# Kernel tuning notes

Measured on AMD Instinct MI355X. Metric: run time of the kernel, lower is better.

Reference implementation:

```python
import jax, jax.numpy as jnp
import numpy as np

B, N, MAX_DEG = 256, 512, 6
F_IN, H = 62, 128  # layers = [62, 128, 128]
NUM_DEG = MAX_DEG + 1  # degree buckets 0..6


def gather_neighbors(atoms, edges, maskvalue):
    # atoms [B,N,F], edges [B,N,D] with -1 padding -> [B,N,D,F]
    idx = jnp.maximum(edges, 0)
    neigh = jax.vmap(lambda a, e: a[e])(atoms, idx)
    return jnp.where(edges[..., None] < 0, jnp.asarray(maskvalue, atoms.dtype), neigh)


def nfp_conv(atoms, edges, W, b):
    # W [NUM_DEG, F_in, F_out], b [NUM_DEG, F_out]
    deg = jnp.sum(edges >= 0, axis=-1)  # [B,N]
    neigh = gather_neighbors(atoms, edges, 0.0)
    summed = neigh.sum(axis=2) + atoms  # include self, [B,N,F_in]
    out = jnp.zeros(summed.shape[:2] + (W.shape[-1],), summed.dtype)
    for d in range(NUM_DEG):  # small fixed set of degree buckets
        h = jax.nn.sigmoid(summed @ W[d] + b[d])
        out = out + h * (deg == d)[..., None].astype(h.dtype)
    return out


def graph_pool(atoms, edges):
    # max over self + neighbors
    neigh = gather_neighbors(atoms, edges, -jnp.inf)
    allf = jnp.concatenate([atoms[:, :, None, :], neigh], axis=2)  # [B,N,D+1,F]
    return allf.max(axis=2)


def setup_inputs() -> dict:
    key = jax.random.key(0)
    ka, ke, km, k0, k1, k2, k3 = jax.random.split(key, 7)
    a = jax.random.normal(ka, (B, N, F_IN), dtype=jnp.float32)
    e = jax.random.randint(ke, (B, N, MAX_DEG), 0, N, dtype=jnp.int32)
    # introduce -1 padding so atoms have varied degrees 0..6
    u = jax.random.uniform(km, (B, N, MAX_DEG))
    e = jnp.where(u < 0.6, e, -1).astype(jnp.int32)
    W0 = jax.random.normal(k0, (NUM_DEG, F_IN, H), dtype=jnp.float32) * 0.1
    b0 = jax.random.normal(k1, (NUM_DEG, H), dtype=jnp.float32) * 0.1
    W1 = jax.random.normal(k2, (NUM_DEG, H, H), dtype=jnp.float32) * 0.1
    b1 = jax.random.normal(k3, (NUM_DEG, H), dtype=jnp.float32) * 0.1
    return {"a": a, "e": e, "W0": W0, "b0": b0, "W1": W1, "b1": b1}


def reference(a, e, W0, b0, W1, b1):
    x = nfp_conv(a, e, W0, b0)
    x = graph_pool(x, e)
    x = nfp_conv(x, e, W1, b1)
    x = graph_pool(x, e)
    return x.sum(axis=1)  # SubgraphSum: [B, H]
```

## Files before the change

kernel.cpp:

```cpp
#include <hip/hip_runtime.h>
#include <math.h>

#define BB 256
#define NN 512
#define DD 6
#define F_IN 62
#define HH 128
#define ND 7
#define TOTAL (BB*NN)
#define G8 8
#define NG 32
#define GOPB 5120
#define MAXSG (NG*GOPB)
#define T128 (MAXSG/128)
#define T64  (MAXSG/64)
#define STG 132

typedef __bf16 bf16x8 __attribute__((ext_vector_type(8)));
typedef float f32x4 __attribute__((ext_vector_type(4)));

__device__ __forceinline__ unsigned short f2bf(float f) {
    unsigned u = __builtin_bit_cast(unsigned, f);
    u = (u + 0x7FFFu + ((u >> 16) & 1u)) >> 16;
    return (unsigned short)u;
}
__device__ __forceinline__ float lo2f(unsigned x) { return __builtin_bit_cast(float, x << 16); }
__device__ __forceinline__ float hi2f(unsigned x) { return __builtin_bit_cast(float, x & 0xFFFF0000u); }

__device__ __forceinline__ uint4 pack8(const float* s) {
    uint4 r;
    r.x = (unsigned)f2bf(s[0]) | ((unsigned)f2bf(s[1]) << 16);
    r.y = (unsigned)f2bf(s[2]) | ((unsigned)f2bf(s[3]) << 16);
    r.z = (unsigned)f2bf(s[4]) | ((unsigned)f2bf(s[5]) << 16);
    r.w = (unsigned)f2bf(s[6]) | ((unsigned)f2bf(s[7]) << 16);
    return r;
}
__device__ __forceinline__ void unpack_add(float* s, uint4 q) {
    s[0] += lo2f(q.x); s[1] += hi2f(q.x); s[2] += lo2f(q.y); s[3] += hi2f(q.y);
    s[4] += lo2f(q.z); s[5] += hi2f(q.z); s[6] += lo2f(q.w); s[7] += hi2f(q.w);
}
__device__ __forceinline__ void unpack_max(float* s, uint4 q) {
    s[0] = fmaxf(s[0], lo2f(q.x)); s[1] = fmaxf(s[1], hi2f(q.x));
    s[2] = fmaxf(s[2], lo2f(q.y)); s[3] = fmaxf(s[3], hi2f(q.y));
    s[4] = fmaxf(s[4], lo2f(q.z)); s[5] = fmaxf(s[5], hi2f(q.z));
    s[6] = fmaxf(s[6], lo2f(q.w)); s[7] = fmaxf(s[7], hi2f(q.w));
}
__device__ __forceinline__ void rowadd62(float* s, const float* r, int kb) {
    float2 z0 = *(const float2*)(r);     s[0] += z0.x; s[1] += z0.y;
    float2 z1 = *(const float2*)(r + 2); s[2] += z1.x; s[3] += z1.y;
    float2 z2 = *(const float2*)(r + 4); s[4] += z2.x; s[5] += z2.y;
    if (kb < 7) { float2 z3 = *(const float2*)(r + 6); s[6] += z3.x; s[7] += z3.y; }
}


__global__ __launch_bounds__(512) void k_hist(const int* __restrict__ e,
                                              int* __restrict__ deg,
                                              int* __restrict__ cnt) {
    __shared__ unsigned int lh[ND];
    const int b = blockIdx.x;
    const int t = threadIdx.x;
    if (t < ND) lh[t] = 0u;
    __syncthreads();
    int d = 0;
#pragma unroll
    for (int j = 0; j < DD; ++j) d += (e[(b * NN + t) * DD + j] >= 0) ? 1 : 0;
    deg[b * NN + t] = d;
    atomicAdd(&lh[d], 1u);
    __syncthreads();
    if (t < ND) cnt[b * 8 + t] = (int)lh[t];
}


__global__ __launch_bounds__(256) void k_scan_grp(const int* __restrict__ cnt,
                                                  int* __restrict__ base_bd,
                                                  int* __restrict__ tdeg64) {
    __shared__ int lc[BB * 8];
    __shared__ int bnd[NG][8];
    const int t = threadIdx.x;
    for (int i = t; i < BB * 8; i += 256) lc[i] = cnt[i];
    __syncthreads();
    if (t < NG) {
        int acc = t * GOPB;
        for (int d = 0; d < ND; ++d) {
            bnd[t][d] = acc;
            for (int b8 = 0; b8 < G8; ++b8) {
                int b = t * G8 + b8;
                base_bd[b * 8 + d] = acc;
                acc += lc[b * 8 + d];
            }
            acc = (acc + 127) & ~127;
        }
        bnd[t][7] = acc;
    }
    __syncthreads();
    for (int i = t; i < T64; i += 256) {
        int g = i / (GOPB / 64);
        int s = i * 64;
        int dd = 0;
        if (s < bnd[g][7]) {
            for (int d = ND - 1; d >= 0; --d) if (s >= bnd[g][d]) { dd = d; break; }
        }
        tdeg64[i] = dd;
    }
}

__global__ __launch_bounds__(512) void k_init_order(int* __restrict__ order) {
    order[blockIdx.x * 512 + threadIdx.x] = -1;
}

__global__ __launch_bounds__(512) void k_scatter(const int* __restrict__ deg,
                                                 const int* __restrict__ base_bd,
                                                 int* __restrict__ order) {
    __shared__ unsigned int rk[ND];
    const int b = blockIdx.x;
    const int t = threadIdx.x;
    if (t < ND) rk[t] = 0u;
    __syncthreads();
    const int u = b * NN + t;
    const int d = deg[u];
    unsigned r = atomicAdd(&rk[d], 1u);
    order[base_bd[b * 8 + d] + (int)r] = u;
}


__global__ void k_prep_wt(const float* __restrict__ W, unsigned short* __restrict__ WT,
                          int F, int K) {
    int n = blockIdx.x;
    int d = blockIdx.y;
    for (int k = threadIdx.x; k < K; k += 64) {
        float v = (k < F) ? W[((size_t)d * F + k) * HH + n] : 0.f;
        WT[((size_t)d * HH + n) * K + k] = f2bf(v);
    }
}


__global__ __launch_bounds__(512, 6)
void k_conv1(const float* __restrict__ a, const int* __restrict__ e,
             const unsigned short* __restrict__ WT, const float* __restrict__ bias,
             const int* __restrict__ order, const int* __restrict__ tdeg64,
             unsigned short* __restrict__ Y) {
    extern __shared__ char smem[];
    unsigned short* Wl = (unsigned short*)smem;
    unsigned short* sA = (unsigned short*)(smem + 16384);
    unsigned short* stg = sA;
    __shared__ int vT[128];

    const int t = threadIdx.x;
    const int l = t & 63;
    const int w = t >> 6;
    const int lr = l & 15;
    const int lq = l >> 4;

    const int x8 = blockIdx.x & 7;
    const int kk0 = blockIdx.x >> 3;
    const int g = x8 * 4 + kk0 / 40;
    const int tile = g * 40 + (kk0 % 40);

    if (order[tile * 128] < 0) return;
    const int d = tdeg64[tile * 2];

    if (t < 128) vT[t] = order[tile * 128 + t];
    for (int u = t; u < 1024; u += 512) {
        const int col = u >> 3, kb = u & 7;
        *(uint4*)&Wl[(col * 8 + (kb ^ (col & 7))) * 8] =
            *(const uint4*)(WT + ((size_t)d * HH + col) * 64 + kb * 8);
    }
    __syncthreads();

    for (int u = t; u < 1024; u += 512) {
        const int n = u >> 3, kb = u & 7;
        const int v = vT[n];
        float s[8] = {0.f, 0.f, 0.f, 0.f, 0.f, 0.f, 0.f, 0.f};
        if (v >= 0) {
            const int nb = v & ~(NN - 1);
            const int* ep = e + (size_t)v * DD;
            rowadd62(s, a + (size_t)v * F_IN + kb * 8, kb);
#pragma unroll
            for (int jj = 0; jj < DD; ++jj) {
                int idx = ep[jj];
                if (idx >= 0) rowadd62(s, a + (size_t)(nb + idx) * F_IN + kb * 8, kb);
            }
        }
        *(uint4*)&sA[(n * 8 + (kb ^ (n & 7))) * 8] = pack8(s);
    }
    __syncthreads();

    const int nrow = w * 16 + lr;
    bf16x8 af[2];
    af[0] = *(const bf16x8*)&sA[(nrow * 8 + ((0 + lq) ^ (nrow & 7))) * 8];
    af[1] = *(const bf16x8*)&sA[(nrow * 8 + ((4 + lq) ^ (nrow & 7))) * 8];

    f32x4 acc[8];
#pragma unroll
    for (int fr = 0; fr < 8; ++fr) {
        const int col = fr * 16 + lr;
        f32x4 z = {0.f, 0.f, 0.f, 0.f};
#pragma unroll
        for (int kk = 0; kk < 2; ++kk) {
            bf16x8 bfr = *(const bf16x8*)&Wl[(col * 8 + ((4 * kk + lq) ^ (col & 7))) * 8];
            z = __builtin_amdgcn_mfma_f32_16x16x32_bf16(af[kk], bfr, z, 0, 0, 0);
        }
        acc[fr] = z;
    }

    __syncthreads();
#pragma unroll
    for (int fr = 0; fr < 8; ++fr) {
        const int col = fr * 16 + lr;
        const float bv = bias[d * HH + col];
#pragma unroll
        for (int r2 = 0; r2 < 4; ++r2) {
            float zz = 1.f / (1.f + __expf(-(acc[fr][r2] + bv)));
            stg[(w * 16 + lq * 4 + r2) * STG + col] = f2bf(zz);
        }
    }
    __syncthreads();
    for (int u = t; u < 2048; u += 512) {
        const int n = u >> 4, c8 = (u & 15) * 8;
        const int v = vT[n];
        if (v >= 0)
            *(uint4*)&Y[(size_t)v * HH + c8] = *(const uint4*)&stg[n * STG + c8];
    }
}


__global__ __launch_bounds__(512, 6)
void k_conv2(const unsigned short* __restrict__ P1, const int* __restrict__ e,
             const unsigned short* __restrict__ WT, const float* __restrict__ bias,
             const int* __restrict__ order, const int* __restrict__ tdeg64,
             unsigned short* __restrict__ Y) {
    extern __shared__ char smem[];
    unsigned short* Wl = (unsigned short*)smem;
    unsigned short* sA = (unsigned short*)(smem + 32768);
    unsigned short* stg = sA;
    __shared__ int vT[64];

    const int t = threadIdx.x;
    const int l = t & 63;
    const int w = t >> 6;
    const int lr = l & 15;
    const int lq = l >> 4;

    const int x8 = blockIdx.x & 7;
    const int kk0 = blockIdx.x >> 3;
    const int g = x8 * 4 + kk0 / 80;
    const int tile = g * 80 + (kk0 % 80);

    if (order[tile * 64] < 0) return;
    const int d = tdeg64[tile];

    if (t < 64) vT[t] = order[tile * 64 + t];
    for (int u = t; u < 2048; u += 512) {
        const int col = u >> 4, kb = u & 15;
        *(uint4*)&Wl[(col * 16 + (kb ^ (col & 7))) * 8] =
            *(const uint4*)(WT + ((size_t)d * HH + col) * 128 + kb * 8);
    }
    __syncthreads();

    for (int u = t; u < 1024; u += 512) {
        const int n = u >> 4, kb = u & 15;
        const int v = vT[n];
        float s[8] = {0.f, 0.f, 0.f, 0.f, 0.f, 0.f, 0.f, 0.f};
        if (v >= 0) {
            const int nb = v & ~(NN - 1);
            const int* ep = e + (size_t)v * DD;
            const unsigned short* base = P1 + kb * 8;
            unpack_add(s, *(const uint4*)(base + (size_t)v * HH));
#pragma unroll
            for (int jj = 0; jj < DD; ++jj) {
                int idx = ep[jj];
                if (idx >= 0) unpack_add(s, *(const uint4*)(base + (size_t)(nb + idx) * HH));
            }
        }
        *(uint4*)&sA[(n * 16 + (kb ^ (n & 7))) * 8] = pack8(s);
    }
    __syncthreads();

    const int nrow = (w & 3) * 16 + lr;
    const int ch = w >> 2;
    bf16x8 af[4];
#pragma unroll
    for (int kk = 0; kk < 4; ++kk)
        af[kk] = *(const bf16x8*)&sA[(nrow * 16 + ((4 * kk + lq) ^ (nrow & 7))) * 8];

    f32x4 acc[4];
#pragma unroll
    for (int fr = 0; fr < 4; ++fr) {
        const int col = ch * 64 + fr * 16 + lr;
        f32x4 z = {0.f, 0.f, 0.f, 0.f};
#pragma unroll
        for (int kk = 0; kk < 4; ++kk) {
            bf16x8 bfr = *(const bf16x8*)&Wl[(col * 16 + ((4 * kk + lq) ^ (col & 7))) * 8];
            z = __builtin_amdgcn_mfma_f32_16x16x32_bf16(af[kk], bfr, z, 0, 0, 0);
        }
        acc[fr] = z;
    }

    __syncthreads();
#pragma unroll
    for (int fr = 0; fr < 4; ++fr) {
        const int col = ch * 64 + fr * 16 + lr;
        const float bv = bias[d * HH + col];
#pragma unroll
        for (int r2 = 0; r2 < 4; ++r2) {
            float zz = 1.f / (1.f + __expf(-(acc[fr][r2] + bv)));
            stg[((w & 3) * 16 + lq * 4 + r2) * STG + col] = f2bf(zz);
        }
    }
    __syncthreads();
    for (int u = t; u < 1024; u += 512) {
        const int n = u >> 4, c8 = (u & 15) * 8;
        const int v = vT[n];
        if (v >= 0)
            *(uint4*)&Y[(size_t)v * HH + c8] = *(const uint4*)&stg[n * STG + c8];
    }
}


__global__ __launch_bounds__(256) void k_pool_bf(const unsigned short* __restrict__ X,
                                                 const int* __restrict__ e,
                                                 unsigned short* __restrict__ P) {
    const int t = threadIdx.x;
    const int u = blockIdx.x * 16 + (t >> 4);
    const int c8 = (t & 15) * 8;
    const int nb = u & ~(NN - 1);
    float m[8];
    {
        uint4 p = *(const uint4*)(X + (size_t)u * HH + c8);
        m[0] = lo2f(p.x); m[1] = hi2f(p.x); m[2] = lo2f(p.y); m[3] = hi2f(p.y);
        m[4] = lo2f(p.z); m[5] = hi2f(p.z); m[6] = lo2f(p.w); m[7] = hi2f(p.w);
    }
#pragma unroll
    for (int jj = 0; jj < DD; ++jj) {
        int idx = e[u * DD + jj];
        if (idx >= 0) unpack_max(m, *(const uint4*)(X + (size_t)(nb + idx) * HH + c8));
    }
    *(uint4*)&P[(size_t)u * HH + c8] = pack8(m);
}


__global__ __launch_bounds__(256) void k_pool_sum_part(const unsigned short* __restrict__ X,
                                                       const int* __restrict__ e,
                                                       float* __restrict__ partial) {
    __shared__ float red[16][HH + 4];
    const int t = threadIdx.x;
    const int b = blockIdx.x >> 5;
    const int chunk = blockIdx.x & 31;
    const int slot = t >> 4;
    const int c8 = (t & 15) * 8;

    const int u = b * NN + chunk * 16 + slot;
    float m[8];
    {
        uint4 p = *(const uint4*)(X + (size_t)u * HH + c8);
        m[0] = lo2f(p.x); m[1] = hi2f(p.x); m[2] = lo2f(p.y); m[3] = hi2f(p.y);
        m[4] = lo2f(p.z); m[5] = hi2f(p.z); m[6] = lo2f(p.w); m[7] = hi2f(p.w);
    }
#pragma unroll
    for (int jj = 0; jj < DD; ++jj) {
        int idx = e[u * DD + jj];
        if (idx >= 0) unpack_max(m, *(const uint4*)(X + (size_t)(b * NN + idx) * HH + c8));
    }
#pragma unroll
    for (int i = 0; i < 8; ++i) red[slot][c8 + i] = m[i];
    __syncthreads();
    if (t < HH) {
        float s = 0.f;
#pragma unroll
        for (int k = 0; k < 16; ++k) s += red[k][t];
        partial[((size_t)b * 32 + chunk) * HH + t] = s;
    }
}

__global__ __launch_bounds__(256) void k_sum_final(const float* __restrict__ partial,
                                                   float* __restrict__ out) {
    int g = blockIdx.x * 256 + threadIdx.x;
    int b = g >> 7;
    int c = g & 127;
    float s = 0.f;
#pragma unroll
    for (int k = 0; k < 32; ++k) s += partial[((size_t)b * 32 + k) * HH + c];
    out[g] = s;
}


extern "C" void kernel_launch(void* const* d_in, const int* in_sizes, int n_in,
                              void* d_out, int out_size, void* d_ws, size_t ws_size,
                              hipStream_t stream) {
    const float* a  = (const float*)d_in[0];
    const int*   e  = (const int*)d_in[1];
    const float* W0 = (const float*)d_in[2];
    const float* b0 = (const float*)d_in[3];
    const float* W1 = (const float*)d_in[4];
    const float* b1 = (const float*)d_in[5];
    float* out = (float*)d_out;

    char* ws = (char*)d_ws;
    const size_t SB = (size_t)TOTAL * HH * 2;
    unsigned short* bufH = (unsigned short*)ws;
    unsigned short* bufP = (unsigned short*)(ws + SB);
    float* partial = (float*)bufP;
    char* dp = ws + 2 * SB;
    unsigned short* WT0 = (unsigned short*)dp;
    unsigned short* WT1 = WT0 + (size_t)ND * HH * 64;
    int* order   = (int*)(WT1 + (size_t)ND * HH * 128);
    int* deg     = order + MAXSG;
    int* cnt     = deg + TOTAL;
    int* base_bd = cnt + BB * 8;
    int* tdeg64  = base_bd + BB * 8;

    hipLaunchKernelGGL(k_hist, dim3(BB), dim3(NN), 0, stream, e, deg, cnt);
    hipLaunchKernelGGL(k_scan_grp, dim3(1), dim3(256), 0, stream, cnt, base_bd, tdeg64);
    hipLaunchKernelGGL(k_init_order, dim3(MAXSG / 512), dim3(512), 0, stream, order);
    hipLaunchKernelGGL(k_scatter, dim3(BB), dim3(NN), 0, stream, deg, base_bd, order);
    hipLaunchKernelGGL(k_prep_wt, dim3(HH, ND), dim3(64), 0, stream, W0, WT0, F_IN, 64);
    hipLaunchKernelGGL(k_prep_wt, dim3(HH, ND), dim3(64), 0, stream, W1, WT1, HH, HH);

    const int lds1 = 16384 + 128 * STG * 2;
    const int lds2 = 32768 + 64 * STG * 2;

    hipLaunchKernelGGL(k_conv1, dim3(T128), dim3(512), lds1, stream,
                       a, e, WT0, b0, order, tdeg64, bufH);
    hipLaunchKernelGGL(k_pool_bf, dim3(TOTAL / 16), dim3(256), 0, stream, bufH, e, bufP);
    hipLaunchKernelGGL(k_conv2, dim3(T64), dim3(512), lds2, stream,
                       bufP, e, WT1, b1, order, tdeg64, bufH);
    hipLaunchKernelGGL(k_pool_sum_part, dim3(BB * 32), dim3(256), 0, stream, bufH, e, partial);
    hipLaunchKernelGGL(k_sum_final, dim3(BB * HH / 256), dim3(256), 0, stream, partial, out);
}
```

Before: 165.1 us.

## Split neighbor gather out of conv GEMMs and merge sort preprocessing kernels

The fused gather+GEMM conv kernels are split into separate gather kernels, which write summed rows in sorted order to a workspace buffer, and GEMM kernels, which load their A fragments straight from that buffer. The four sort and histogram preprocessing kernels are merged into one per-group kernel using LDS atomics, and the two weight-prep launches are combined into one. The aim is to free the GEMM kernels from latency-bound gathers and LDS staging, and to cut launch count. In exchange, the gathered intermediate makes an extra round trip through global memory and two more launches are added.

```diff
diff --git a/kernel.cpp b/kernel.cpp
--- a/kernel.cpp
+++ b/kernel.cpp
@@ -12,8 +12,8 @@
 #define NG 32
 #define GOPB 5120
 #define MAXSG (NG*GOPB)
-#define T128 (MAXSG/128)
-#define T64  (MAXSG/64)
+#define T128G 40
+#define T64G 80
 #define STG 132
 
 typedef __bf16 bf16x8 __attribute__((ext_vector_type(8)));
@@ -53,96 +53,131 @@
 }
 
 
-__global__ __launch_bounds__(512) void k_hist(const int* __restrict__ e,
-                                              int* __restrict__ deg,
-                                              int* __restrict__ cnt) {
-    __shared__ unsigned int lh[ND];
-    const int b = blockIdx.x;
+__global__ __launch_bounds__(1024)
+void k_sort_grp(const int* __restrict__ e, int* __restrict__ order,
+                int* __restrict__ tdeg64) {
+    __shared__ int cnt[G8][8];
+    __shared__ int base[G8][8];
+    __shared__ int bnd[8];
+    __shared__ short degl[G8 * NN];
+    const int g = blockIdx.x;
     const int t = threadIdx.x;
-    if (t < ND) lh[t] = 0u;
-    __syncthreads();
-    int d = 0;
-#pragma unroll
-    for (int j = 0; j < DD; ++j) d += (e[(b * NN + t) * DD + j] >= 0) ? 1 : 0;
-    deg[b * NN + t] = d;
-    atomicAdd(&lh[d], 1u);
-    __syncthreads();
-    if (t < ND) cnt[b * 8 + t] = (int)lh[t];
-}
-
-
-__global__ __launch_bounds__(256) void k_scan_grp(const int* __restrict__ cnt,
-                                                  int* __restrict__ base_bd,
-                                                  int* __restrict__ tdeg64) {
-    __shared__ int lc[BB * 8];
-    __shared__ int bnd[NG][8];
-    const int t = threadIdx.x;
-    for (int i = t; i < BB * 8; i += 256) lc[i] = cnt[i];
-    __syncthreads();
-    if (t < NG) {
-        int acc = t * GOPB;
+    if (t < 64) ((int*)cnt)[t] = 0;
+    for (int i = t; i < GOPB; i += 1024) order[g * GOPB + i] = -1;
+    __syncthreads();
+#pragma unroll
+    for (int q = 0; q < 4; ++q) {
+        const int n = q * 1024 + t;
+        const int b8 = n >> 9, nn = n & (NN - 1);
+        const int u = (g * G8 + b8) * NN + nn;
+        int d = 0;
+#pragma unroll
+        for (int j = 0; j < DD; ++j) d += (e[u * DD + j] >= 0) ? 1 : 0;
+        degl[n] = (short)d;
+        atomicAdd(&cnt[b8][d], 1);
+    }
+    __syncthreads();
+    if (t == 0) {
+        int acc = g * GOPB;
         for (int d = 0; d < ND; ++d) {
-            bnd[t][d] = acc;
-            for (int b8 = 0; b8 < G8; ++b8) {
-                int b = t * G8 + b8;
-                base_bd[b * 8 + d] = acc;
-                acc += lc[b * 8 + d];
-            }
+            bnd[d] = acc;
+            for (int b8 = 0; b8 < G8; ++b8) { base[b8][d] = acc; acc += cnt[b8][d]; }
             acc = (acc + 127) & ~127;
         }
-        bnd[t][7] = acc;
-    }
-    __syncthreads();
-    for (int i = t; i < T64; i += 256) {
-        int g = i / (GOPB / 64);
-        int s = i * 64;
+        bnd[7] = acc;
+    }
+    __syncthreads();
+    for (int i = t; i < T64G; i += 1024) {
+        const int s = g * GOPB + i * 64;
         int dd = 0;
-        if (s < bnd[g][7]) {
-            for (int d = ND - 1; d >= 0; --d) if (s >= bnd[g][d]) { dd = d; break; }
+        if (s < bnd[7]) {
+            for (int d = ND - 1; d >= 0; --d) if (s >= bnd[d]) { dd = d; break; }
         }
-        tdeg64[i] = dd;
-    }
-}
-
-__global__ __launch_bounds__(512) void k_init_order(int* __restrict__ order) {
-    order[blockIdx.x * 512 + threadIdx.x] = -1;
-}
-
-__global__ __launch_bounds__(512) void k_scatter(const int* __restrict__ deg,
-                                                 const int* __restrict__ base_bd,
-                                                 int* __restrict__ order) {
-    __shared__ unsigned int rk[ND];
-    const int b = blockIdx.x;
-    const int t = threadIdx.x;
-    if (t < ND) rk[t] = 0u;
-    __syncthreads();
-    const int u = b * NN + t;
-    const int d = deg[u];
-    unsigned r = atomicAdd(&rk[d], 1u);
-    order[base_bd[b * 8 + d] + (int)r] = u;
-}
-
-
-__global__ void k_prep_wt(const float* __restrict__ W, unsigned short* __restrict__ WT,
-                          int F, int K) {
-    int n = blockIdx.x;
-    int d = blockIdx.y;
-    for (int k = threadIdx.x; k < K; k += 64) {
-        float v = (k < F) ? W[((size_t)d * F + k) * HH + n] : 0.f;
-        WT[((size_t)d * HH + n) * K + k] = f2bf(v);
-    }
+        tdeg64[g * T64G + i] = dd;
+    }
+    __syncthreads();
+#pragma unroll
+    for (int q = 0; q < 4; ++q) {
+        const int n = q * 1024 + t;
+        const int b8 = n >> 9, nn = n & (NN - 1);
+        const int slot = atomicAdd(&base[b8][degl[n]], 1);
+        order[slot] = (g * G8 + b8) * NN + nn;
+    }
+}
+
+
+__global__ void k_prep_w2(const float* __restrict__ W0, unsigned short* __restrict__ WT0,
+                          const float* __restrict__ W1, unsigned short* __restrict__ WT1) {
+    const int n = blockIdx.x;
+    const int d = blockIdx.y;
+    for (int k = threadIdx.x; k < 64; k += 64) {
+        float v = (k < F_IN) ? W0[((size_t)d * F_IN + k) * HH + n] : 0.f;
+        WT0[((size_t)d * HH + n) * 64 + k] = f2bf(v);
+    }
+    for (int k = threadIdx.x; k < 128; k += 64)
+        WT1[((size_t)d * HH + n) * 128 + k] = f2bf(W1[((size_t)d * HH + k) * HH + n]);
+}
+
+
+__global__ __launch_bounds__(512)
+void k_gather1(const float* __restrict__ a, const int* __restrict__ e,
+               const int* __restrict__ order, unsigned short* __restrict__ S1) {
+    const int bi = blockIdx.x;
+    const int x8 = bi & 7;
+    const int r = bi >> 3;
+    const int g = x8 * 4 + r / 80;
+    const int blk = r % 80;
+    const int slot = g * GOPB + blk * 64 + (threadIdx.x >> 3);
+    const int kb = threadIdx.x & 7;
+    const int v = order[slot];
+    if (v < 0) return;
+    const int* ep = e + (size_t)v * DD;
+    const int nb = v & ~(NN - 1);
+    float s[8] = {0.f, 0.f, 0.f, 0.f, 0.f, 0.f, 0.f, 0.f};
+    rowadd62(s, a + (size_t)v * F_IN + kb * 8, kb);
+#pragma unroll
+    for (int jj = 0; jj < DD; ++jj) {
+        int idx = ep[jj];
+        if (idx >= 0) rowadd62(s, a + (size_t)(nb + idx) * F_IN + kb * 8, kb);
+    }
+    *(uint4*)(S1 + (size_t)slot * 64 + kb * 8) = pack8(s);
+}
+
+
+__global__ __launch_bounds__(512)
+void k_gather2(const unsigned short* __restrict__ P1, const int* __restrict__ e,
+               const int* __restrict__ order, unsigned short* __restrict__ S2) {
+    const int bi = blockIdx.x;
+    const int x8 = bi & 7;
+    const int r = bi >> 3;
+    const int g = x8 * 4 + r / 160;
+    const int blk = r % 160;
+    const int slot = g * GOPB + blk * 32 + (threadIdx.x >> 4);
+    const int kb = threadIdx.x & 15;
+    const int v = order[slot];
+    if (v < 0) return;
+    const int* ep = e + (size_t)v * DD;
+    const int nb = v & ~(NN - 1);
+    const unsigned short* base = P1 + kb * 8;
+    float s[8] = {0.f, 0.f, 0.f, 0.f, 0.f, 0.f, 0.f, 0.f};
+    unpack_add(s, *(const uint4*)(base + (size_t)v * HH));
+#pragma unroll
+    for (int jj = 0; jj < DD; ++jj) {
+        int idx = ep[jj];
+        if (idx >= 0) unpack_add(s, *(const uint4*)(base + (size_t)(nb + idx) * HH));
+    }
+    *(uint4*)(S2 + (size_t)slot * HH + kb * 8) = pack8(s);
 }
 
 
 __global__ __launch_bounds__(512, 6)
-void k_conv1(const float* __restrict__ a, const int* __restrict__ e,
+void k_gemm1(const unsigned short* __restrict__ S,
              const unsigned short* __restrict__ WT, const float* __restrict__ bias,
              const int* __restrict__ order, const int* __restrict__ tdeg64,
              unsigned short* __restrict__ Y) {
     extern __shared__ char smem[];
-    unsigned short* Wl = (unsigned short*)smem;
-    unsigned short* sA = (unsigned short*)(smem + 16384);
-    unsigned short* stg = sA;
+    unsigned short* Wl  = (unsigned short*)smem;
+    unsigned short* stg = (unsigned short*)(smem + 16384);
     __shared__ int vT[128];
 
     const int t = threadIdx.x;
@@ -151,15 +186,21 @@
     const int lr = l & 15;
     const int lq = l >> 4;
 
-    const int x8 = blockIdx.x & 7;
-    const int kk0 = blockIdx.x >> 3;
-    const int g = x8 * 4 + kk0 / 40;
-    const int tile = g * 40 + (kk0 % 40);
-
-    if (order[tile * 128] < 0) return;
-    const int d = tdeg64[tile * 2];
-
-    if (t < 128) vT[t] = order[tile * 128 + t];
+    const int bi = blockIdx.x;
+    const int x8 = bi & 7;
+    const int r = bi >> 3;
+    const int g = x8 * 4 + r / T128G;
+    const int ti = r % T128G;
+    const int sbase = g * GOPB + ti * 128;
+    if (order[sbase] < 0) return;
+    const int d = tdeg64[g * T64G + ti * 2];
+
+    if (t < 128) vT[t] = order[sbase + t];
+
+    const unsigned short* sp = S + (size_t)(sbase + w * 16 + lr) * 64;
+    bf16x8 af0 = *(const bf16x8*)(sp + lq * 8);
+    bf16x8 af1 = *(const bf16x8*)(sp + (lq + 4) * 8);
+
     for (int u = t; u < 1024; u += 512) {
         const int col = u >> 3, kb = u & 7;
         *(uint4*)&Wl[(col * 8 + (kb ^ (col & 7))) * 8] =
@@ -167,39 +208,15 @@
     }
     __syncthreads();
 
-    for (int u = t; u < 1024; u += 512) {
-        const int n = u >> 3, kb = u & 7;
-        const int v = vT[n];
-        float s[8] = {0.f, 0.f, 0.f, 0.f, 0.f, 0.f, 0.f, 0.f};
-        if (v >= 0) {
-            const int nb = v & ~(NN - 1);
-            const int* ep = e + (size_t)v * DD;
-            rowadd62(s, a + (size_t)v * F_IN + kb * 8, kb);
-#pragma unroll
-            for (int jj = 0; jj < DD; ++jj) {
-                int idx = ep[jj];
-                if (idx >= 0) rowadd62(s, a + (size_t)(nb + idx) * F_IN + kb * 8, kb);
-            }
-        }
-        *(uint4*)&sA[(n * 8 + (kb ^ (n & 7))) * 8] = pack8(s);
-    }
-    __syncthreads();
-
-    const int nrow = w * 16 + lr;
-    bf16x8 af[2];
-    af[0] = *(const bf16x8*)&sA[(nrow * 8 + ((0 + lq) ^ (nrow & 7))) * 8];
-    af[1] = *(const bf16x8*)&sA[(nrow * 8 + ((4 + lq) ^ (nrow & 7))) * 8];
-
     f32x4 acc[8];
 #pragma unroll
     for (int fr = 0; fr < 8; ++fr) {
         const int col = fr * 16 + lr;
         f32x4 z = {0.f, 0.f, 0.f, 0.f};
-#pragma unroll
-        for (int kk = 0; kk < 2; ++kk) {
-            bf16x8 bfr = *(const bf16x8*)&Wl[(col * 8 + ((4 * kk + lq) ^ (col & 7))) * 8];
-            z = __builtin_amdgcn_mfma_f32_16x16x32_bf16(af[kk], bfr, z, 0, 0, 0);
-        }
+        bf16x8 b0 = *(const bf16x8*)&Wl[(col * 8 + ((0 + lq) ^ (col & 7))) * 8];
+        z = __builtin_amdgcn_mfma_f32_16x16x32_bf16(af0, b0, z, 0, 0, 0);
+        bf16x8 b1 = *(const bf16x8*)&Wl[(col * 8 + ((4 + lq) ^ (col & 7))) * 8];
+        z = __builtin_amdgcn_mfma_f32_16x16x32_bf16(af1, b1, z, 0, 0, 0);
         acc[fr] = z;
     }
 
@@ -225,14 +242,13 @@
 
 
 __global__ __launch_bounds__(512, 6)
-void k_conv2(const unsigned short* __restrict__ P1, const int* __restrict__ e,
+void k_gemm2(const unsigned short* __restrict__ S,
              const unsigned short* __restrict__ WT, const float* __restrict__ bias,
              const int* __restrict__ order, const int* __restrict__ tdeg64,
              unsigned short* __restrict__ Y) {
     extern __shared__ char smem[];
-    unsigned short* Wl = (unsigned short*)smem;
-    unsigned short* sA = (unsigned short*)(smem + 32768);
-    unsigned short* stg = sA;
+    unsigned short* Wl  = (unsigned short*)smem;
+    unsigned short* stg = (unsigned short*)(smem + 32768);
     __shared__ int vT[64];
 
     const int t = threadIdx.x;
@@ -241,47 +257,32 @@
     const int lr = l & 15;
     const int lq = l >> 4;
 
-    const int x8 = blockIdx.x & 7;
-    const int kk0 = blockIdx.x >> 3;
-    const int g = x8 * 4 + kk0 / 80;
-    const int tile = g * 80 + (kk0 % 80);
-
-    if (order[tile * 64] < 0) return;
-    const int d = tdeg64[tile];
-
-    if (t < 64) vT[t] = order[tile * 64 + t];
+    const int bi = blockIdx.x;
+    const int x8 = bi & 7;
+    const int r = bi >> 3;
+    const int g = x8 * 4 + r / T64G;
+    const int ti = r % T64G;
+    const int sbase = g * GOPB + ti * 64;
+    if (order[sbase] < 0) return;
+    const int d = tdeg64[g * T64G + ti];
+
+    if (t < 64) vT[t] = order[sbase + t];
+
+    const int nrow = (w & 3) * 16 + lr;
+    const int ch = w >> 2;
+
+    const unsigned short* sp = S + (size_t)(sbase + nrow) * 128;
+    bf16x8 af[4];
+#pragma unroll
+    for (int kk = 0; kk < 4; ++kk)
+        af[kk] = *(const bf16x8*)(sp + (lq + 4 * kk) * 8);
+
     for (int u = t; u < 2048; u += 512) {
         const int col = u >> 4, kb = u & 15;
         *(uint4*)&Wl[(col * 16 + (kb ^ (col & 7))) * 8] =
             *(const uint4*)(WT + ((size_t)d * HH + col) * 128 + kb * 8);
     }
     __syncthreads();
-
-    for (int u = t; u < 1024; u += 512) {
-        const int n = u >> 4, kb = u & 15;
-        const int v = vT[n];
-        float s[8] = {0.f, 0.f, 0.f, 0.f, 0.f, 0.f, 0.f, 0.f};
-        if (v >= 0) {
-            const int nb = v & ~(NN - 1);
-            const int* ep = e + (size_t)v * DD;
-            const unsigned short* base = P1 + kb * 8;
-            unpack_add(s, *(const uint4*)(base + (size_t)v * HH));
-#pragma unroll
-            for (int jj = 0; jj < DD; ++jj) {
-                int idx = ep[jj];
-                if (idx >= 0) unpack_add(s, *(const uint4*)(base + (size_t)(nb + idx) * HH));
-            }
-        }
-        *(uint4*)&sA[(n * 16 + (kb ^ (n & 7))) * 8] = pack8(s);
-    }
-    __syncthreads();
-
-    const int nrow = (w & 3) * 16 + lr;
-    const int ch = w >> 2;
-    bf16x8 af[4];
-#pragma unroll
-    for (int kk = 0; kk < 4; ++kk)
-        af[kk] = *(const bf16x8*)&sA[(nrow * 16 + ((4 * kk + lq) ^ (nrow & 7))) * 8];
 
     f32x4 acc[4];
 #pragma unroll
@@ -374,13 +375,13 @@
 
 __global__ __launch_bounds__(256) void k_sum_final(const float* __restrict__ partial,
                                                    float* __restrict__ out) {
-    int g = blockIdx.x * 256 + threadIdx.x;
-    int b = g >> 7;
-    int c = g & 127;
+    int gi = blockIdx.x * 256 + threadIdx.x;
+    int b = gi >> 7;
+    int c = gi & 127;
     float s = 0.f;
 #pragma unroll
     for (int k = 0; k < 32; ++k) s += partial[((size_t)b * 32 + k) * HH + c];
-    out[g] = s;
+    out[gi] = s;
 }
 
 
@@ -396,34 +397,31 @@
     float* out = (float*)d_out;
 
     char* ws = (char*)d_ws;
-    const size_t SB = (size_t)TOTAL * HH * 2;
-    unsigned short* bufH = (unsigned short*)ws;
-    unsigned short* bufP = (unsigned short*)(ws + SB);
-    float* partial = (float*)bufP;
-    char* dp = ws + 2 * SB;
+    unsigned short* S1 = (unsigned short*)ws;
+    unsigned short* h1 = (unsigned short*)(ws + 20971520);
+    unsigned short* p1 = (unsigned short*)(ws + 54525952);
+    unsigned short* S2 = (unsigned short*)ws;
+    unsigned short* h2 = (unsigned short*)(ws + 41943040);
+    float* partial = (float*)ws;
+    char* dp = ws + 88080384;
     unsigned short* WT0 = (unsigned short*)dp;
     unsigned short* WT1 = WT0 + (size_t)ND * HH * 64;
-    int* order   = (int*)(WT1 + (size_t)ND * HH * 128);
-    int* deg     = order + MAXSG;
-    int* cnt     = deg + TOTAL;
-    int* base_bd = cnt + BB * 8;
-    int* tdeg64  = base_bd + BB * 8;
-
-    hipLaunchKernelGGL(k_hist, dim3(BB), dim3(NN), 0, stream, e, deg, cnt);
-    hipLaunchKernelGGL(k_scan_grp, dim3(1), dim3(256), 0, stream, cnt, base_bd, tdeg64);
-    hipLaunchKernelGGL(k_init_order, dim3(MAXSG / 512), dim3(512), 0, stream, order);
-    hipLaunchKernelGGL(k_scatter, dim3(BB), dim3(NN), 0, stream, deg, base_bd, order);
-    hipLaunchKernelGGL(k_prep_wt, dim3(HH, ND), dim3(64), 0, stream, W0, WT0, F_IN, 64);
-    hipLaunchKernelGGL(k_prep_wt, dim3(HH, ND), dim3(64), 0, stream, W1, WT1, HH, HH);
+    int* order  = (int*)(WT1 + (size_t)ND * HH * 128);
+    int* tdeg64 = order + MAXSG;
+
+    hipLaunchKernelGGL(k_sort_grp, dim3(NG), dim3(1024), 0, stream, e, order, tdeg64);
+    hipLaunchKernelGGL(k_prep_w2, dim3(HH, ND), dim3(64), 0, stream, W0, WT0, W1, WT1);
 
     const int lds1 = 16384 + 128 * STG * 2;
     const int lds2 = 32768 + 64 * STG * 2;
 
-    hipLaunchKernelGGL(k_conv1, dim3(T128), dim3(512), lds1, stream,
-                       a, e, WT0, b0, order, tdeg64, bufH);
-    hipLaunchKernelGGL(k_pool_bf, dim3(TOTAL / 16), dim3(256), 0, stream, bufH, e, bufP);
-    hipLaunchKernelGGL(k_conv2, dim3(T64), dim3(512), lds2, stream,
-                       bufP, e, WT1, b1, order, tdeg64, bufH);
-    hipLaunchKernelGGL(k_pool_sum_part, dim3(BB * 32), dim3(256), 0, stream, bufH, e, partial);
+    hipLaunchKernelGGL(k_gather1, dim3(NG * 80), dim3(512), 0, stream, a, e, order, S1);
+    hipLaunchKernelGGL(k_gemm1, dim3(NG * T128G), dim3(512), lds1, stream,
+                       S1, WT0, b0, order, tdeg64, h1);
+    hipLaunchKernelGGL(k_pool_bf, dim3(TOTAL / 16), dim3(256), 0, stream, h1, e, p1);
+    hipLaunchKernelGGL(k_gather2, dim3(NG * 160), dim3(512), 0, stream, p1, e, order, S2);
+    hipLaunchKernelGGL(k_gemm2, dim3(NG * T64G), dim3(512), lds2, stream,
+                       S2, WT1, b1, order, tdeg64, h2);
+    hipLaunchKernelGGL(k_pool_sum_part, dim3(BB * 32), dim3(256), 0, stream, h2, e, partial);
     hipLaunchKernelGGL(k_sum_final, dim3(BB * HH / 256), dim3(256), 0, stream, partial, out);
 }
```

New measurement: 162.2 us. About the same (-1.7%).
